# Performance work log

Measured on AMD Instinct MI355X. Metric: run time of the kernel, lower is better.

The kernel has to match this reference:

```python
import jax, jax.numpy as jnp
import numpy as np

ND, NT, B = 16384, 16384, 4096
FD, FT, C = 256, 256, 768


def _gat(x_src, x_dst, ei, Ws, Wd, a_s, a_d, b, num_dst, self_loops):
    """PyG GATConv, heads=1: per-edge attention softmax over incoming edges."""
    if self_loops:
        loops = jnp.arange(num_dst, dtype=ei.dtype)
        ei = jnp.concatenate([ei, jnp.stack([loops, loops])], axis=1)
    src, dst = ei[0], ei[1]
    hs = x_src @ Ws                                   # [Ns, C]
    hd = x_dst @ Wd                                   # [Ndst, C]
    e = jax.nn.leaky_relu((hs @ a_s)[src] + (hd @ a_d)[dst], 0.2)   # [E]
    m = jax.ops.segment_max(e, dst, num_segments=num_dst)
    p = jnp.exp(e - m[dst])
    s = jax.ops.segment_sum(p, dst, num_segments=num_dst)
    alpha = p / (s[dst] + 1e-16)
    out = jax.ops.segment_sum(hs[src] * alpha[:, None], dst, num_segments=num_dst)
    return out + b


def _l2norm(x):
    n = jnp.linalg.norm(x, axis=1, keepdims=True)
    return x / jnp.maximum(n, 1e-12)


def setup_inputs() -> dict:
    ks = iter(jax.random.split(jax.random.key(0), 64))
    def nrm(shape, fan_in=None):
        s = 1.0 if fan_in is None else (1.0 / fan_in) ** 0.5
        return jax.random.normal(next(ks), shape, jnp.float32) * s
    inp = {}
    inp["x_drug"] = nrm((ND, FD))
    inp["x_target"] = nrm((NT, FT))
    inp["cell_features"] = nrm((B, 890))
    for et, fs, fd in (("dd", FD, FD), ("dt", FD, FT), ("tt", FT, FT)):
        inp[f"W_src_{et}"] = nrm((fs, C), fs)
        inp[f"W_dst_{et}"] = nrm((fd, C), fd)
        inp[f"a_src_{et}"] = nrm((C,), C)
        inp[f"a_dst_{et}"] = nrm((C,), C)
        inp[f"b_{et}"] = jnp.zeros((C,), jnp.float32)
    for name, fi, fo in (("red1", 890, 2048), ("red2", 2048, 512), ("red3", 512, 2 * C),
                         ("r2a", 4 * C, 2048), ("r2b", 2048, 512), ("r2c", 512, C), ("cls", C, 2)):
        inp[f"{name}_w"] = nrm((fi, fo), fi)
        inp[f"{name}_b"] = jnp.zeros((fo,), jnp.float32)
    inp["drug1_id"] = jax.random.randint(next(ks), (B,), 0, ND)
    inp["drug2_id"] = jax.random.randint(next(ks), (B,), 0, ND)
    inp["ei_dd"] = jax.random.randint(next(ks), (2, 131072), 0, ND)
    inp["ei_dt"] = jnp.stack([jax.random.randint(next(ks), (262144,), 0, ND),
                              jax.random.randint(next(ks), (262144,), 0, NT)])
    inp["ei_tt"] = jax.random.randint(next(ks), (2, 262144), 0, NT)
    return inp


def reference(x_drug, x_target, cell_features,
              W_src_dd, W_dst_dd, a_src_dd, a_dst_dd, b_dd,
              W_src_dt, W_dst_dt, a_src_dt, a_dst_dt, b_dt,
              W_src_tt, W_dst_tt, a_src_tt, a_dst_tt, b_tt,
              red1_w, red1_b, red2_w, red2_b, red3_w, red3_b,
              r2a_w, r2a_b, r2b_w, r2b_b, r2c_w, r2c_b,
              cls_w, cls_b,
              drug1_id, drug2_id, ei_dd, ei_dt, ei_tt):
    # HeteroConv (aggr='sum') followed by per-type ReLU, num_layers=1
    drug = jax.nn.relu(_gat(x_drug, x_drug, ei_dd,
                            W_src_dd, W_dst_dd, a_src_dd, a_dst_dd, b_dd, ND, True))
    target = jax.nn.relu(
        _gat(x_drug, x_target, ei_dt, W_src_dt, W_dst_dt, a_src_dt, a_dst_dt, b_dt, NT, False)
        + _gat(x_target, x_target, ei_tt, W_src_tt, W_dst_tt, a_src_tt, a_dst_tt, b_tt, NT, True))
    del target  # with num_layers=1 the target embeddings never feed the output (faithful)
    d1 = drug[drug1_id]
    d2 = drug[drug2_id]
    cell = _l2norm(cell_features)
    cell = jax.nn.relu(cell @ red1_w + red1_b)
    cell = jax.nn.relu(cell @ red2_w + red2_b)
    cell = jax.nn.relu(cell @ red3_w + red3_b)          # [B, 2*C]
    hidden = _l2norm(jnp.concatenate([d1, d2, cell], axis=1))  # [B, 4*C]
    hidden = jax.nn.relu(hidden @ r2a_w + r2a_b)
    hidden = jax.nn.relu(hidden @ r2b_w + r2b_b)
    hidden = jax.nn.relu(hidden @ r2c_w + r2c_b)
    return hidden @ cls_w + cls_b                       # [B, 2]
```

## Files before the change

### kernel.cpp

```cpp
#include <hip/hip_runtime.h>
#include <cstdint>

#define ND 16384
#define BATCH 4096
#define CDIM 768
#define E_DD 131072
#define FD 256

typedef unsigned short u16;
typedef u16 u16x4 __attribute__((ext_vector_type(4)));
typedef u16 u16x8 __attribute__((ext_vector_type(8)));
typedef short s16x8 __attribute__((ext_vector_type(8)));
typedef float f32x4 __attribute__((ext_vector_type(4)));

__device__ __forceinline__ u16 f2bf(float x) {
  union { float f; uint32_t u; } v; v.f = x;
  uint32_t r = v.u + 0x7fffu + ((v.u >> 16) & 1u);
  return (u16)(r >> 16);
}
__device__ __forceinline__ float bf2f(u16 h) {
  union { float f; uint32_t u; } v; v.u = ((uint32_t)h) << 16;
  return v.f;
}
__device__ __forceinline__ uint32_t split2p(float x) {
  u16 h = f2bf(x);
  u16 l = f2bf(x - bf2f(h));
  return ((uint32_t)h << 16) | l;
}

#define KP 40

template <int KS, int OUT_BF16, int RELU, int BIAS, int ASPLIT, int ALO, int BLO>
__device__ __forceinline__ void gemm_core(
    int bx, int by, int bz,
    const float* __restrict__ Af,
    const u16* __restrict__ Ahi, const u16* __restrict__ Alo,
    const u16* __restrict__ Bhi, const u16* __restrict__ Blo,
    const float* __restrict__ bias,
    float* __restrict__ Cf, u16* __restrict__ Chi,
    int M, int N, int K, u16* AsB, u16* BsB) {
  constexpr int MT = 4, NT = 4;
  constexpr int BM = 128, BN = 128;
  constexpr int ASEG = BM / 64;
  constexpr int BSEG = BN / 64;

  const int t = threadIdx.x;
  const int bm0 = bx * BM, bn0 = by * BN;
  const int wid = t >> 6, lane = t & 63;
  const int quad = lane >> 4, l16 = lane & 15;
  const int wm0 = (wid >> 1) * (MT * 16);
  const int wn0 = (wid & 1) * (NT * 16);

  const int chunk = K / KS;
  const int kbeg = (KS > 1) ? bz * chunk : 0;
  const int kend = kbeg + chunk;

  auto As = [&](int a, int r, int k) -> u16& { return AsB[(a * BM + r) * KP + k]; };
  auto Bs = [&](int a, int r, int k) -> u16& { return BsB[(a * BN + r) * KP + k]; };

  f32x4 acc[MT][NT];
#pragma unroll
  for (int i = 0; i < MT; ++i)
#pragma unroll
    for (int j = 0; j < NT; ++j) acc[i][j] = (f32x4){0.f, 0.f, 0.f, 0.f};

  u16x8 pAh[ASEG], pAl[ASEG], pBh[BSEG], pBl[BSEG];

  auto loadA = [&](int c, int kk) {
    int s = t + 256 * c, row = s >> 2, kq = (s & 3) * 8;
    size_t off = (size_t)(bm0 + row) * K + kk + kq;
    if (ASPLIT) {
      f32x4 v0 = *(const f32x4*)(Af + off);
      f32x4 v1 = *(const f32x4*)(Af + off + 4);
      u16x8 h, l;
#pragma unroll
      for (int e = 0; e < 4; ++e) {
        uint32_t p = split2p(v0[e]);
        h[e] = (u16)(p >> 16); l[e] = (u16)(p & 0xffffu);
        uint32_t q = split2p(v1[e]);
        h[e + 4] = (u16)(q >> 16); l[e + 4] = (u16)(q & 0xffffu);
      }
      pAh[c] = h; pAl[c] = l;
    } else {
      pAh[c] = *(const u16x8*)(Ahi + off);
      if (ALO) pAl[c] = *(const u16x8*)(Alo + off);
    }
  };
  auto loadB = [&](int c, int kk) {
    int s = t + 256 * c, row = s >> 2, kq = (s & 3) * 8;
    size_t off = (size_t)(bn0 + row) * K + kk + kq;
    pBh[c] = *(const u16x8*)(Bhi + off);
    if (BLO) pBl[c] = *(const u16x8*)(Blo + off);
  };

#pragma unroll
  for (int c = 0; c < ASEG; ++c) loadA(c, kbeg);
#pragma unroll
  for (int c = 0; c < BSEG; ++c) loadB(c, kbeg);

  for (int k0 = kbeg;;) {
    __syncthreads();
#pragma unroll
    for (int c = 0; c < ASEG; ++c) {
      int s = t + 256 * c, row = s >> 2, kq = (s & 3) * 8;
      *(u16x8*)&As(0, row, kq) = pAh[c];
      if (ALO) *(u16x8*)&As(1, row, kq) = pAl[c];
    }
#pragma unroll
    for (int c = 0; c < BSEG; ++c) {
      int s = t + 256 * c, row = s >> 2, kq = (s & 3) * 8;
      *(u16x8*)&Bs(0, row, kq) = pBh[c];
      if (BLO) *(u16x8*)&Bs(1, row, kq) = pBl[c];
    }
    __syncthreads();

    int kn = k0 + 32;
    if (kn < kend) {
#pragma unroll
      for (int c = 0; c < ASEG; ++c) loadA(c, kn);
#pragma unroll
      for (int c = 0; c < BSEG; ++c) loadB(c, kn);
    }

    s16x8 ah[MT], al[MT], bh[NT], bl[NT];
#pragma unroll
    for (int mi = 0; mi < MT; ++mi) {
      ah[mi] = *(const s16x8*)&As(0, wm0 + mi * 16 + l16, quad * 8);
      if (ALO) al[mi] = *(const s16x8*)&As(1, wm0 + mi * 16 + l16, quad * 8);
    }
#pragma unroll
    for (int ni = 0; ni < NT; ++ni) {
      bh[ni] = *(const s16x8*)&Bs(0, wn0 + ni * 16 + l16, quad * 8);
      if (BLO) bl[ni] = *(const s16x8*)&Bs(1, wn0 + ni * 16 + l16, quad * 8);
    }
#pragma unroll
    for (int mi = 0; mi < MT; ++mi)
#pragma unroll
      for (int ni = 0; ni < NT; ++ni) {
        acc[mi][ni] = __builtin_amdgcn_mfma_f32_16x16x32_bf16(
            ah[mi], bh[ni], acc[mi][ni], 0, 0, 0);
        if (BLO)
          acc[mi][ni] = __builtin_amdgcn_mfma_f32_16x16x32_bf16(
              ah[mi], bl[ni], acc[mi][ni], 0, 0, 0);
        if (ALO)
          acc[mi][ni] = __builtin_amdgcn_mfma_f32_16x16x32_bf16(
              al[mi], bh[ni], acc[mi][ni], 0, 0, 0);
      }
    k0 = kn;
    if (k0 >= kend) break;
  }

  float* Cp = (KS > 1) ? Cf + (size_t)bz * M * N : Cf;
#pragma unroll
  for (int mi = 0; mi < MT; ++mi) {
#pragma unroll
    for (int ni = 0; ni < NT; ++ni) {
      int row = bm0 + wm0 + mi * 16 + quad * 4;
      int col = bn0 + wn0 + ni * 16 + l16;
      float bv = BIAS ? bias[col] : 0.f;
#pragma unroll
      for (int r = 0; r < 4; ++r) {
        float v = acc[mi][ni][r] + bv;
        if (RELU) v = fmaxf(v, 0.f);
        size_t o = (size_t)(row + r) * N + col;
        if (OUT_BF16) Chi[o] = f2bf(v);
        else Cp[o] = v;
      }
    }
  }
}

template <int KS, int OUT_BF16, int RELU, int BIAS, int ASPLIT, int ALO, int BLO>
__global__ __launch_bounds__(256) void mfma_gemm(
    const float* __restrict__ Af,
    const u16* __restrict__ Ahi, const u16* __restrict__ Alo,
    const u16* __restrict__ Bhi, const u16* __restrict__ Blo,
    const float* __restrict__ bias,
    float* __restrict__ Cf, u16* __restrict__ Chi,
    int M, int N, int K) {
  __shared__ __align__(16) u16 AsB[(ALO ? 2 : 1) * 128 * KP];
  __shared__ __align__(16) u16 BsB[(BLO ? 2 : 1) * 128 * KP];
  gemm_core<KS, OUT_BF16, RELU, BIAS, ASPLIT, ALO, BLO>(
      blockIdx.x, blockIdx.y, (KS > 1) ? (int)blockIdx.z : 0,
      Af, Ahi, Alo, Bhi, Blo, bias, Cf, Chi, M, N, K, AsB, BsB);
}

__global__ __launch_bounds__(256) void dual_gemm_red1_hs(
    const u16* __restrict__ cn, const u16* __restrict__ r1T,
    const float* __restrict__ red1_b, u16* __restrict__ c1,
    const float* __restrict__ xd, const u16* __restrict__ wsrcT,
    u16* __restrict__ hs) {
  __shared__ __align__(16) u16 AsB[2 * 128 * KP];
  __shared__ __align__(16) u16 BsB[128 * KP];
  int b = blockIdx.x;
  if (b < 512) {
    gemm_core<1, 1, 1, 1, 0, 0, 0>(b & 31, b >> 5, 0, nullptr, cn, nullptr,
                                   r1T, nullptr, red1_b, nullptr, c1,
                                   BATCH, 2048, 896, AsB, BsB);
  } else {
    int b2 = b - 512;
    gemm_core<1, 1, 0, 0, 1, 1, 0>(b2 & 127, b2 >> 7, 0, xd, nullptr, nullptr,
                                   wsrcT, nullptr, nullptr, nullptr, hs,
                                   ND, CDIM, FD, AsB, BsB);
  }
}

template <int KS>
__global__ void reduce_split_ks(const float* __restrict__ P,
                                const float* __restrict__ bias,
                                u16* __restrict__ Chi, int M, int N) {
  int i = blockIdx.x * 256 + threadIdx.x;
  int total = (M * N) >> 2;
  if (i >= total) return;
  f32x4 s = ((const f32x4*)P)[i];
#pragma unroll
  for (int z = 1; z < KS; ++z) s += ((const f32x4*)P)[(size_t)z * total + i];
  int col = (i * 4) % N;
  f32x4 bv = *(const f32x4*)(bias + col);
  u16x4 h;
#pragma unroll
  for (int e = 0; e < 4; ++e) h[e] = f2bf(fmaxf(s[e] + bv[e], 0.f));
  *(u16x4*)&Chi[i * 4] = h;
}

__global__ void reduce_cls(const float* __restrict__ P,
                           const float* __restrict__ bias,
                           const float* __restrict__ clsw,
                           const float* __restrict__ clsb,
                           float* __restrict__ out) {
  int row = blockIdx.x * 4 + (threadIdx.x >> 6);
  int lane = threadIdx.x & 63;
  const f32x4* p0 = (const f32x4*)(P + (size_t)row * CDIM);
  const f32x4* p1 = (const f32x4*)(P + (size_t)BATCH * CDIM + (size_t)row * CDIM);
  float s0 = 0.f, s1 = 0.f;
#pragma unroll
  for (int i = 0; i < 3; ++i) {
    int c4 = lane + 64 * i;
    f32x4 a = p0[c4] + p1[c4];
    f32x4 bv = *(const f32x4*)(bias + c4 * 4);
#pragma unroll
    for (int e = 0; e < 4; ++e) {
      float h = fmaxf(a[e] + bv[e], 0.f);
      int c = c4 * 4 + e;
      s0 = fmaf(h, clsw[c * 2 + 0], s0);
      s1 = fmaf(h, clsw[c * 2 + 1], s1);
    }
  }
#pragma unroll
  for (int m = 32; m; m >>= 1) {
    s0 += __shfl_xor(s0, m);
    s1 += __shfl_xor(s1, m);
  }
  if (lane == 0) {
    out[row * 2 + 0] = s0 + clsb[0];
    out[row * 2 + 1] = s1 + clsb[1];
  }
}

struct TDesc {
  const float* W;
  u16* Th;
  int K, N, Kpad, start;
};
struct TPack { TDesc d[7]; };

__global__ void multi_transpose(TPack p) {
  __shared__ float tile[32][33];
  int b = blockIdx.x;
  int mi = 0;
#pragma unroll
  for (int i = 1; i < 7; ++i)
    if (b >= p.d[i].start) mi = i;
  TDesc dd = p.d[mi];
  int rel = b - dd.start;
  int tilesX = dd.Kpad / 32;
  int k0 = (rel % tilesX) * 32, n0 = (rel / tilesX) * 32;
  int tx = threadIdx.x, ty = threadIdx.y;
#pragma unroll
  for (int i = 0; i < 4; ++i) {
    int k = k0 + ty + 8 * i, n = n0 + tx;
    tile[ty + 8 * i][tx] = (k < dd.K && n < dd.N) ? dd.W[(size_t)k * dd.N + n] : 0.f;
  }
  __syncthreads();
#pragma unroll
  for (int i = 0; i < 4; ++i) {
    int n = n0 + ty + 8 * i, k = k0 + tx;
    if (n < dd.N) dd.Th[(size_t)n * dd.Kpad + k] = f2bf(tile[tx][ty + 8 * i]);
  }
}

__global__ void wvec_kernel(const float* __restrict__ Wsrc,
                            const float* __restrict__ Wdst,
                            const float* __restrict__ a_s,
                            const float* __restrict__ a_d,
                            float* __restrict__ wsv, float* __restrict__ wdv) {
  int k = blockIdx.x;
  int t = threadIdx.x;
  __shared__ float rs[256], rd[256];
  float s = 0.f, d = 0.f;
  for (int c = t; c < CDIM; c += 256) {
    s += Wsrc[(size_t)k * CDIM + c] * a_s[c];
    d += Wdst[(size_t)k * CDIM + c] * a_d[c];
  }
  rs[t] = s; rd[t] = d;
  __syncthreads();
  for (int st = 128; st; st >>= 1) {
    if (t < st) { rs[t] += rs[t + st]; rd[t] += rd[t + st]; }
    __syncthreads();
  }
  if (t == 0) { wsv[k] = rs[0]; wdv[k] = rd[0]; }
}

__global__ void esed_kernel(const float* __restrict__ x,
                            const float* __restrict__ wsv,
                            const float* __restrict__ wdv,
                            float* __restrict__ es, float* __restrict__ ed) {
  int i = blockIdx.x * 256 + threadIdx.x;
  int lane = threadIdx.x & 63;
  int row = i >> 6;
  int c4 = lane * 4;
  f32x4 v = ((const f32x4*)x)[i];
  f32x4 ws = *(const f32x4*)(wsv + c4);
  f32x4 wd = *(const f32x4*)(wdv + c4);
  float a = v[0] * ws[0] + v[1] * ws[1] + v[2] * ws[2] + v[3] * ws[3];
  float b = v[0] * wd[0] + v[1] * wd[1] + v[2] * wd[2] + v[3] * wd[3];
#pragma unroll
  for (int m = 32; m; m >>= 1) {
    a += __shfl_xor(a, m);
    b += __shfl_xor(b, m);
  }
  if (lane == 0) { es[row] = a; ed[row] = b; }
}

__global__ void init_csr(int* counts, int* mask, int* cnt) {
  int i = blockIdx.x * 256 + threadIdx.x;
  if (i < ND) { counts[i] = 1; mask[i] = 0; }
  if (i == 0) *cnt = 0;
}
__global__ void mark_kernel(const int* __restrict__ d1, const int* __restrict__ d2,
                            int* mask) {
  int i = blockIdx.x * 256 + threadIdx.x;
  if (i < BATCH) {
    mask[d1[i]] = 1;
    mask[d2[i]] = 1;
  }
}
__global__ void compact_kernel(const int* __restrict__ mask, int* cnt, int* list) {
  int i = blockIdx.x * 256 + threadIdx.x;
  if (i < ND && mask[i]) {
    int pos = atomicAdd(cnt, 1);
    list[pos] = i;
  }
}

__global__ void count_edges(const int* __restrict__ dst, int* counts) {
  int e = blockIdx.x * 256 + threadIdx.x;
  if (e < E_DD) atomicAdd(&counts[dst[e]], 1);
}
__global__ void scan_kernel(const int* __restrict__ counts, int* __restrict__ offsets,
                            int* __restrict__ cursor, int* __restrict__ slots) {
  __shared__ int part[512];
  int t = threadIdx.x;
  int base = t * 32;
  int s = 0;
  for (int i = 0; i < 32; ++i) s += counts[base + i];
  part[t] = s;
  __syncthreads();
  if (t == 0) {
    int run = 0;
    for (int i = 0; i < 512; ++i) { int tmp = part[i]; part[i] = run; run += tmp; }
    offsets[ND] = run;
  }
  __syncthreads();
  int run = part[t];
  for (int i = 0; i < 32; ++i) {
    int d = base + i;
    offsets[d] = run;
    slots[run] = d;
    cursor[d] = run + 1;
    run += counts[d];
  }
}
__global__ void scatter_edges(const int* __restrict__ src, const int* __restrict__ dst,
                              int* cursor, int* slots) {
  int e = blockIdx.x * 256 + threadIdx.x;
  if (e < E_DD) {
    int pos = atomicAdd(&cursor[dst[e]], 1);
    slots[pos] = src[e];
  }
}

__global__ __launch_bounds__(256) void gat_aggregate(
    const u16* __restrict__ hs, const float* __restrict__ es,
    const float* __restrict__ ed, const int* __restrict__ offsets,
    const int* __restrict__ slots, const float* __restrict__ bias,
    const int* __restrict__ list, const int* __restrict__ cnt,
    u16* __restrict__ out) {
  int idx = blockIdx.x * 4 + (threadIdx.x >> 6);
  if (idx >= *cnt) return;
  int d = list[idx];
  int lane = threadIdx.x & 63;
  int beg = offsets[d], end = offsets[d + 1];
  float edv = ed[d];
  float mx = -1e30f;
  for (int j = beg + lane; j < end; j += 64) {
    float e = es[slots[j]] + edv;
    e = e >= 0.f ? e : 0.2f * e;
    mx = fmaxf(mx, e);
  }
#pragma unroll
  for (int m = 32; m; m >>= 1) mx = fmaxf(mx, __shfl_xor(mx, m));
  float sm = 0.f;
  for (int j = beg + lane; j < end; j += 64) {
    float e = es[slots[j]] + edv;
    e = e >= 0.f ? e : 0.2f * e;
    sm += expf(e - mx);
  }
#pragma unroll
  for (int m = 32; m; m >>= 1) sm += __shfl_xor(sm, m);
  float inv = 1.f / (sm + 1e-16f);
  int c8 = lane * 8;
  int c4 = 512 + lane * 4;
  float a8[8] = {};
  float a4[4] = {};
  for (int j = beg; j < end; ++j) {
    int srcn = slots[j];
    float e = es[srcn] + edv;
    e = e >= 0.f ? e : 0.2f * e;
    float alpha = expf(e - mx) * inv;
    const u16* hrow = hs + (size_t)srcn * CDIM;
    u16x8 r8 = *(const u16x8*)(hrow + c8);
    u16x4 r4 = *(const u16x4*)(hrow + c4);
#pragma unroll
    for (int e2 = 0; e2 < 8; ++e2) a8[e2] = fmaf(alpha, bf2f(r8[e2]), a8[e2]);
#pragma unroll
    for (int e2 = 0; e2 < 4; ++e2) a4[e2] = fmaf(alpha, bf2f(r4[e2]), a4[e2]);
  }
  u16* orow = out + (size_t)d * CDIM;
  u16x8 o8;
  u16x4 o4;
#pragma unroll
  for (int e2 = 0; e2 < 8; ++e2) o8[e2] = f2bf(fmaxf(a8[e2] + bias[c8 + e2], 0.f));
#pragma unroll
  for (int e2 = 0; e2 < 4; ++e2) o4[e2] = f2bf(fmaxf(a4[e2] + bias[c4 + e2], 0.f));
  *(u16x8*)(orow + c8) = o8;
  *(u16x4*)(orow + c4) = o4;
}

__global__ void l2norm_bf16(const float* __restrict__ in, u16* __restrict__ hi,
                            int L, int Lp) {
  int row = blockIdx.x;
  int t = threadIdx.x;
  __shared__ float red[256];
  const float* irow = in + (size_t)row * L;
  float s = 0.f;
  for (int c = t; c < L; c += 256) { float v = irow[c]; s += v * v; }
  red[t] = s;
  __syncthreads();
  for (int st = 128; st; st >>= 1) {
    if (t < st) red[t] += red[t + st];
    __syncthreads();
  }
  float inv = 1.f / fmaxf(sqrtf(red[0]), 1e-12f);
  for (int c = t; c < Lp; c += 256) {
    float v = (c < L) ? irow[c] * inv : 0.f;
    hi[(size_t)row * Lp + c] = f2bf(v);
  }
}

__global__ __launch_bounds__(256) void hidden_build_bf16(
    const u16* __restrict__ drug, const u16* __restrict__ c3,
    const int* __restrict__ d1, const int* __restrict__ d2,
    u16* __restrict__ hhi) {
  int row = blockIdx.x;
  int t = threadIdx.x;
  const u16* s1 = drug + (size_t)d1[row] * CDIM;
  const u16* s2 = drug + (size_t)d2[row] * CDIM;
  const u16* s3 = c3 + (size_t)row * (2 * CDIM);
  float vals[12];
  float ss = 0.f;
#pragma unroll
  for (int i = 0; i < 12; ++i) {
    int c = t + 256 * i;
    float v;
    if (i < 3)      v = bf2f(s1[c]);
    else if (i < 6) v = bf2f(s2[c - CDIM]);
    else            v = bf2f(s3[c - 2 * CDIM]);
    vals[i] = v;
    ss += v * v;
  }
  __shared__ float red[256];
  red[t] = ss;
  __syncthreads();
  for (int st = 128; st; st >>= 1) {
    if (t < st) red[t] += red[t + st];
    __syncthreads();
  }
  float inv = 1.f / fmaxf(sqrtf(red[0]), 1e-12f);
  u16* hrow_h = hhi + (size_t)row * (4 * CDIM);
#pragma unroll
  for (int i = 0; i < 12; ++i) hrow_h[t + 256 * i] = f2bf(vals[i] * inv);
}

extern "C" void kernel_launch(void* const* d_in, const int* in_sizes, int n_in,
                              void* d_out, int out_size, void* d_ws, size_t ws_size,
                              hipStream_t stream) {
  const float* x_drug   = (const float*)d_in[0];
  const float* cellf    = (const float*)d_in[2];
  const float* W_src_dd = (const float*)d_in[3];
  const float* W_dst_dd = (const float*)d_in[4];
  const float* a_src_dd = (const float*)d_in[5];
  const float* a_dst_dd = (const float*)d_in[6];
  const float* b_dd     = (const float*)d_in[7];
  const float* red1_w = (const float*)d_in[18];
  const float* red1_b = (const float*)d_in[19];
  const float* red2_w = (const float*)d_in[20];
  const float* red2_b = (const float*)d_in[21];
  const float* red3_w = (const float*)d_in[22];
  const float* red3_b = (const float*)d_in[23];
  const float* r2a_w  = (const float*)d_in[24];
  const float* r2a_b  = (const float*)d_in[25];
  const float* r2b_w  = (const float*)d_in[26];
  const float* r2b_b  = (const float*)d_in[27];
  const float* r2c_w  = (const float*)d_in[28];
  const float* r2c_b  = (const float*)d_in[29];
  const float* cls_w  = (const float*)d_in[30];
  const float* cls_b  = (const float*)d_in[31];
  const int* drug1_id = (const int*)d_in[32];
  const int* drug2_id = (const int*)d_in[33];
  const int* ei_dd    = (const int*)d_in[34];
  float* out = (float*)d_out;

  const int* dd_src = ei_dd;
  const int* dd_dst = ei_dd + E_DD;

  char* w = (char*)d_ws;
  size_t off = 0;
  auto alloc = [&](size_t bytes) -> char* {
    char* p = w + off;
    off = (off + bytes + 255) & ~(size_t)255;
    return p;
  };
  u16* hs   = (u16*)alloc((size_t)ND * CDIM * 2);
  u16* drug = (u16*)alloc((size_t)ND * CDIM * 2);
  u16* c3   = (u16*)alloc((size_t)BATCH * 2 * CDIM * 2);
  float* P  = (float*)alloc((size_t)4 * BATCH * 512 * 4);
  u16* hid_hi = hs;
  u16* cn_hi = (u16*)alloc((size_t)BATCH * 896 * 2);
  u16* c1_hi = (u16*)alloc((size_t)BATCH * 2048 * 2);
  u16* c2_hi = (u16*)alloc((size_t)BATCH * 512 * 2);
  u16* wsrcT_hi = (u16*)alloc((size_t)CDIM * FD * 2);
  u16* r1T_hi = (u16*)alloc((size_t)2048 * 896 * 2);
  u16* r2T_hi = (u16*)alloc((size_t)512 * 2048 * 2);
  u16* r3T_hi = (u16*)alloc((size_t)1536 * 512 * 2);
  u16* raT_hi = (u16*)alloc((size_t)2048 * 3072 * 2);
  u16* rbT_hi = (u16*)alloc((size_t)512 * 2048 * 2);
  u16* rcT_hi = (u16*)alloc((size_t)768 * 512 * 2);
  float* es  = (float*)alloc((size_t)ND * 4);
  float* ed  = (float*)alloc((size_t)ND * 4);
  float* wsv = (float*)alloc(FD * 4);
  float* wdv = (float*)alloc(FD * 4);
  int* counts  = (int*)alloc((size_t)ND * 4);
  int* offsets = (int*)alloc((size_t)(ND + 1) * 4);
  int* cursor  = (int*)alloc((size_t)ND * 4);
  int* slots   = (int*)alloc((size_t)(E_DD + ND) * 4);
  int* mask    = (int*)alloc((size_t)ND * 4);
  int* list    = (int*)alloc((size_t)ND * 4);
  int* cnt     = (int*)alloc(256);
  (void)ws_size; (void)n_in; (void)in_sizes; (void)out_size;

  TPack tp;
  tp.d[0] = {W_src_dd, wsrcT_hi, 256, 768, 256, 0};
  tp.d[1] = {red1_w, r1T_hi, 890, 2048, 896, 192};
  tp.d[2] = {red2_w, r2T_hi, 2048, 512, 2048, 1984};
  tp.d[3] = {red3_w, r3T_hi, 512, 1536, 512, 3008};
  tp.d[4] = {r2a_w, raT_hi, 3072, 2048, 3072, 3776};
  tp.d[5] = {r2b_w, rbT_hi, 2048, 512, 2048, 9920};
  tp.d[6] = {r2c_w, rcT_hi, 512, 768, 512, 10944};
  multi_transpose<<<11328, dim3(32, 8), 0, stream>>>(tp);

  wvec_kernel<<<FD, 256, 0, stream>>>(W_src_dd, W_dst_dd, a_src_dd, a_dst_dd, wsv, wdv);
  esed_kernel<<<ND * FD / 1024, 256, 0, stream>>>(x_drug, wsv, wdv, es, ed);
  init_csr<<<ND / 256, 256, 0, stream>>>(counts, mask, cnt);
  mark_kernel<<<BATCH / 256, 256, 0, stream>>>(drug1_id, drug2_id, mask);
  compact_kernel<<<ND / 256, 256, 0, stream>>>(mask, cnt, list);
  l2norm_bf16<<<BATCH, 256, 0, stream>>>(cellf, cn_hi, 890, 896);

  dual_gemm_red1_hs<<<1280, 256, 0, stream>>>(cn_hi, r1T_hi, red1_b, c1_hi,
                                              x_drug, wsrcT_hi, hs);

  mfma_gemm<4, 0, 0, 0, 0, 0, 0><<<dim3(BATCH / 128, 512 / 128, 4), 256, 0, stream>>>(
      nullptr, c1_hi, nullptr, r2T_hi, nullptr, nullptr, P, nullptr, BATCH, 512, 2048);
  reduce_split_ks<4><<<BATCH * 512 / 1024, 256, 0, stream>>>(P, red2_b, c2_hi, BATCH, 512);
  mfma_gemm<1, 1, 1, 1, 0, 0, 0><<<dim3(BATCH / 128, 1536 / 128), 256, 0, stream>>>(
      nullptr, c2_hi, nullptr, r3T_hi, nullptr, red3_b, nullptr, c3, BATCH, 1536, 512);

  count_edges<<<E_DD / 256, 256, 0, stream>>>(dd_dst, counts);
  scan_kernel<<<1, 512, 0, stream>>>(counts, offsets, cursor, slots);
  scatter_edges<<<E_DD / 256, 256, 0, stream>>>(dd_src, dd_dst, cursor, slots);
  gat_aggregate<<<ND / 4, 256, 0, stream>>>(hs, es, ed, offsets, slots, b_dd, list, cnt, drug);

  hidden_build_bf16<<<BATCH, 256, 0, stream>>>(drug, c3, drug1_id, drug2_id, hid_hi);

  mfma_gemm<1, 1, 1, 1, 0, 0, 0><<<dim3(BATCH / 128, 2048 / 128), 256, 0, stream>>>(
      nullptr, hid_hi, nullptr, raT_hi, nullptr, r2a_b, nullptr, c1_hi, BATCH, 2048, 3072);
  mfma_gemm<4, 0, 0, 0, 0, 0, 0><<<dim3(BATCH / 128, 512 / 128, 4), 256, 0, stream>>>(
      nullptr, c1_hi, nullptr, rbT_hi, nullptr, nullptr, P, nullptr, BATCH, 512, 2048);
  reduce_split_ks<4><<<BATCH * 512 / 1024, 256, 0, stream>>>(P, r2b_b, c2_hi, BATCH, 512);
  mfma_gemm<2, 0, 0, 0, 0, 0, 0><<<dim3(BATCH / 128, CDIM / 128, 2), 256, 0, stream>>>(
      nullptr, c2_hi, nullptr, rcT_hi, nullptr, nullptr, P, nullptr, BATCH, CDIM, 512);
  reduce_cls<<<BATCH / 4, 256, 0, stream>>>(P, r2c_b, cls_w, cls_b, out);
}
```

Before: 483.6 us.

## Stage plain bf16 GEMM tiles via direct global-to-LDS loads with double buffering

For GEMM instantiations without fp32 splitting or low-part operands, tiles are now copied straight from global memory into LDS with global_load_lds. This skips the register round trip, and a double-buffered scheme needs only one barrier per k-step. The LDS layout drops the padding (stride 32 instead of 40), which may add bank conflicts on the fragment reads. Shared memory in the dual kernel is merged into one buffer sized for both paths. There is no explicit wait on the async LDS loads before the barrier, which risks reading data that has not arrived.

```diff
diff --git a/kernel.cpp b/kernel.cpp
--- a/kernel.cpp
+++ b/kernel.cpp
@@ -27,6 +27,11 @@
   u16 l = f2bf(x - bf2f(h));
   return ((uint32_t)h << 16) | l;
 }
+
+#define GLOAD_LDS16(gp, lp)                                                   \
+  __builtin_amdgcn_global_load_lds(                                           \
+      (__attribute__((address_space(1))) void*)(gp),                          \
+      (__attribute__((address_space(3))) void*)(lp), 16, 0, 0)
 
 #define KP 40
 
@@ -43,6 +48,7 @@
   constexpr int BM = 128, BN = 128;
   constexpr int ASEG = BM / 64;
   constexpr int BSEG = BN / 64;
+  constexpr bool DIRECT = (ASPLIT == 0 && ALO == 0 && BLO == 0);
 
   const int t = threadIdx.x;
   const int bm0 = bx * BM, bn0 = by * BN;
@@ -55,99 +61,167 @@
   const int kbeg = (KS > 1) ? bz * chunk : 0;
   const int kend = kbeg + chunk;
 
-  auto As = [&](int a, int r, int k) -> u16& { return AsB[(a * BM + r) * KP + k]; };
-  auto Bs = [&](int a, int r, int k) -> u16& { return BsB[(a * BN + r) * KP + k]; };
-
   f32x4 acc[MT][NT];
 #pragma unroll
   for (int i = 0; i < MT; ++i)
 #pragma unroll
     for (int j = 0; j < NT; ++j) acc[i][j] = (f32x4){0.f, 0.f, 0.f, 0.f};
 
-  u16x8 pAh[ASEG], pAl[ASEG], pBh[BSEG], pBl[BSEG];
-
-  auto loadA = [&](int c, int kk) {
-    int s = t + 256 * c, row = s >> 2, kq = (s & 3) * 8;
-    size_t off = (size_t)(bm0 + row) * K + kk + kq;
-    if (ASPLIT) {
-      f32x4 v0 = *(const f32x4*)(Af + off);
-      f32x4 v1 = *(const f32x4*)(Af + off + 4);
-      u16x8 h, l;
-#pragma unroll
-      for (int e = 0; e < 4; ++e) {
-        uint32_t p = split2p(v0[e]);
-        h[e] = (u16)(p >> 16); l[e] = (u16)(p & 0xffffu);
-        uint32_t q = split2p(v1[e]);
-        h[e + 4] = (u16)(q >> 16); l[e + 4] = (u16)(q & 0xffffu);
-      }
-      pAh[c] = h; pAl[c] = l;
-    } else {
-      pAh[c] = *(const u16x8*)(Ahi + off);
-      if (ALO) pAl[c] = *(const u16x8*)(Alo + off);
+  if constexpr (DIRECT) {
+    auto stage = [&](int buf, int kk) {
+#pragma unroll
+      for (int c = 0; c < ASEG; ++c) {
+        int s = t + 256 * c;
+        size_t goff = (size_t)(bm0 + (s >> 2)) * K + kk + (s & 3) * 8;
+        int lofs = __builtin_amdgcn_readfirstlane(
+            buf * (2 * BM * 32) + 0 * 0 + (wid * 64 + 256 * c) * 8);
+        GLOAD_LDS16(Ahi + goff, AsB + (buf * (BM * 32) + (lofs - buf * (2 * BM * 32))));
+      }
+#pragma unroll
+      for (int c = 0; c < BSEG; ++c) {
+        int s = t + 256 * c;
+        size_t goff = (size_t)(bn0 + (s >> 2)) * K + kk + (s & 3) * 8;
+        int lofs = __builtin_amdgcn_readfirstlane((wid * 64 + 256 * c) * 8);
+        GLOAD_LDS16(Bhi + goff, BsB + buf * (BN * 32) + lofs);
+      }
+    };
+    auto stageA = [&](int buf, int kk) {
+#pragma unroll
+      for (int c = 0; c < ASEG; ++c) {
+        int s = t + 256 * c;
+        size_t goff = (size_t)(bm0 + (s >> 2)) * K + kk + (s & 3) * 8;
+        int lofs = __builtin_amdgcn_readfirstlane((wid * 64 + 256 * c) * 8);
+        GLOAD_LDS16(Ahi + goff, AsB + buf * (BM * 32) + lofs);
+      }
+    };
+    auto stageB = [&](int buf, int kk) {
+#pragma unroll
+      for (int c = 0; c < BSEG; ++c) {
+        int s = t + 256 * c;
+        size_t goff = (size_t)(bn0 + (s >> 2)) * K + kk + (s & 3) * 8;
+        int lofs = __builtin_amdgcn_readfirstlane((wid * 64 + 256 * c) * 8);
+        GLOAD_LDS16(Bhi + goff, BsB + buf * (BN * 32) + lofs);
+      }
+    };
+    (void)stage;
+    stageA(0, kbeg);
+    stageB(0, kbeg);
+    int cur = 0;
+    for (int k0 = kbeg;;) {
+      __syncthreads();
+      int kn = k0 + 32;
+      if (kn < kend) {
+        stageA(cur ^ 1, kn);
+        stageB(cur ^ 1, kn);
+      }
+      const u16* Ab = AsB + cur * (BM * 32);
+      const u16* Bb = BsB + cur * (BN * 32);
+      s16x8 ah[MT], bh[NT];
+#pragma unroll
+      for (int mi = 0; mi < MT; ++mi)
+        ah[mi] = *(const s16x8*)(Ab + (wm0 + mi * 16 + l16) * 32 + quad * 8);
+#pragma unroll
+      for (int ni = 0; ni < NT; ++ni)
+        bh[ni] = *(const s16x8*)(Bb + (wn0 + ni * 16 + l16) * 32 + quad * 8);
+#pragma unroll
+      for (int mi = 0; mi < MT; ++mi)
+#pragma unroll
+        for (int ni = 0; ni < NT; ++ni)
+          acc[mi][ni] = __builtin_amdgcn_mfma_f32_16x16x32_bf16(
+              ah[mi], bh[ni], acc[mi][ni], 0, 0, 0);
+      k0 = kn;
+      cur ^= 1;
+      if (k0 >= kend) break;
     }
-  };
-  auto loadB = [&](int c, int kk) {
-    int s = t + 256 * c, row = s >> 2, kq = (s & 3) * 8;
-    size_t off = (size_t)(bn0 + row) * K + kk + kq;
-    pBh[c] = *(const u16x8*)(Bhi + off);
-    if (BLO) pBl[c] = *(const u16x8*)(Blo + off);
-  };
-
-#pragma unroll
-  for (int c = 0; c < ASEG; ++c) loadA(c, kbeg);
-#pragma unroll
-  for (int c = 0; c < BSEG; ++c) loadB(c, kbeg);
-
-  for (int k0 = kbeg;;) {
-    __syncthreads();
-#pragma unroll
-    for (int c = 0; c < ASEG; ++c) {
+  } else {
+    auto As = [&](int a, int r, int k) -> u16& { return AsB[(a * BM + r) * KP + k]; };
+    auto Bs = [&](int a, int r, int k) -> u16& { return BsB[(a * BN + r) * KP + k]; };
+
+    u16x8 pAh[ASEG], pAl[ASEG], pBh[BSEG], pBl[BSEG];
+
+    auto loadA = [&](int c, int kk) {
       int s = t + 256 * c, row = s >> 2, kq = (s & 3) * 8;
-      *(u16x8*)&As(0, row, kq) = pAh[c];
-      if (ALO) *(u16x8*)&As(1, row, kq) = pAl[c];
+      size_t off = (size_t)(bm0 + row) * K + kk + kq;
+      if (ASPLIT) {
+        f32x4 v0 = *(const f32x4*)(Af + off);
+        f32x4 v1 = *(const f32x4*)(Af + off + 4);
+        u16x8 h, l;
+#pragma unroll
+        for (int e = 0; e < 4; ++e) {
+          uint32_t p = split2p(v0[e]);
+          h[e] = (u16)(p >> 16); l[e] = (u16)(p & 0xffffu);
+          uint32_t q = split2p(v1[e]);
+          h[e + 4] = (u16)(q >> 16); l[e + 4] = (u16)(q & 0xffffu);
+        }
+        pAh[c] = h; pAl[c] = l;
+      } else {
+        pAh[c] = *(const u16x8*)(Ahi + off);
+        if (ALO) pAl[c] = *(const u16x8*)(Alo + off);
+      }
+    };
+    auto loadB = [&](int c, int kk) {
+      int s = t + 256 * c, row = s >> 2, kq = (s & 3) * 8;
+      size_t off = (size_t)(bn0 + row) * K + kk + kq;
+      pBh[c] = *(const u16x8*)(Bhi + off);
+      if (BLO) pBl[c] = *(const u16x8*)(Blo + off);
+    };
+
+#pragma unroll
+    for (int c = 0; c < ASEG; ++c) loadA(c, kbeg);
+#pragma unroll
+    for (int c = 0; c < BSEG; ++c) loadB(c, kbeg);
+
+    for (int k0 = kbeg;;) {
+      __syncthreads();
+#pragma unroll
+      for (int c = 0; c < ASEG; ++c) {
+        int s = t + 256 * c, row = s >> 2, kq = (s & 3) * 8;
+        *(u16x8*)&As(0, row, kq) = pAh[c];
+        if (ALO) *(u16x8*)&As(1, row, kq) = pAl[c];
+      }
+#pragma unroll
+      for (int c = 0; c < BSEG; ++c) {
+        int s = t + 256 * c, row = s >> 2, kq = (s & 3) * 8;
+        *(u16x8*)&Bs(0, row, kq) = pBh[c];
+        if (BLO) *(u16x8*)&Bs(1, row, kq) = pBl[c];
+      }
+      __syncthreads();
+
+      int kn = k0 + 32;
+      if (kn < kend) {
+#pragma unroll
+        for (int c = 0; c < ASEG; ++c) loadA(c, kn);
+#pragma unroll
+        for (int c = 0; c < BSEG; ++c) loadB(c, kn);
+      }
+
+      s16x8 ah[MT], al[MT], bh[NT], bl[NT];
+#pragma unroll
+      for (int mi = 0; mi < MT; ++mi) {
+        ah[mi] = *(const s16x8*)&As(0, wm0 + mi * 16 + l16, quad * 8);
+        if (ALO) al[mi] = *(const s16x8*)&As(1, wm0 + mi * 16 + l16, quad * 8);
+      }
+#pragma unroll
+      for (int ni = 0; ni < NT; ++ni) {
+        bh[ni] = *(const s16x8*)&Bs(0, wn0 + ni * 16 + l16, quad * 8);
+        if (BLO) bl[ni] = *(const s16x8*)&Bs(1, wn0 + ni * 16 + l16, quad * 8);
+      }
+#pragma unroll
+      for (int mi = 0; mi < MT; ++mi)
+#pragma unroll
+        for (int ni = 0; ni < NT; ++ni) {
+          acc[mi][ni] = __builtin_amdgcn_mfma_f32_16x16x32_bf16(
+              ah[mi], bh[ni], acc[mi][ni], 0, 0, 0);
+          if (BLO)
+            acc[mi][ni] = __builtin_amdgcn_mfma_f32_16x16x32_bf16(
+                ah[mi], bl[ni], acc[mi][ni], 0, 0, 0);
+          if (ALO)
+            acc[mi][ni] = __builtin_amdgcn_mfma_f32_16x16x32_bf16(
+                al[mi], bh[ni], acc[mi][ni], 0, 0, 0);
+        }
+      k0 = kn;
+      if (k0 >= kend) break;
     }
-#pragma unroll
-    for (int c = 0; c < BSEG; ++c) {
-      int s = t + 256 * c, row = s >> 2, kq = (s & 3) * 8;
-      *(u16x8*)&Bs(0, row, kq) = pBh[c];
-      if (BLO) *(u16x8*)&Bs(1, row, kq) = pBl[c];
-    }
-    __syncthreads();
-
-    int kn = k0 + 32;
-    if (kn < kend) {
-#pragma unroll
-      for (int c = 0; c < ASEG; ++c) loadA(c, kn);
-#pragma unroll
-      for (int c = 0; c < BSEG; ++c) loadB(c, kn);
-    }
-
-    s16x8 ah[MT], al[MT], bh[NT], bl[NT];
-#pragma unroll
-    for (int mi = 0; mi < MT; ++mi) {
-      ah[mi] = *(const s16x8*)&As(0, wm0 + mi * 16 + l16, quad * 8);
-      if (ALO) al[mi] = *(const s16x8*)&As(1, wm0 + mi * 16 + l16, quad * 8);
-    }
-#pragma unroll
-    for (int ni = 0; ni < NT; ++ni) {
-      bh[ni] = *(const s16x8*)&Bs(0, wn0 + ni * 16 + l16, quad * 8);
-      if (BLO) bl[ni] = *(const s16x8*)&Bs(1, wn0 + ni * 16 + l16, quad * 8);
-    }
-#pragma unroll
-    for (int mi = 0; mi < MT; ++mi)
-#pragma unroll
-      for (int ni = 0; ni < NT; ++ni) {
-        acc[mi][ni] = __builtin_amdgcn_mfma_f32_16x16x32_bf16(
-            ah[mi], bh[ni], acc[mi][ni], 0, 0, 0);
-        if (BLO)
-          acc[mi][ni] = __builtin_amdgcn_mfma_f32_16x16x32_bf16(
-              ah[mi], bl[ni], acc[mi][ni], 0, 0, 0);
-        if (ALO)
-          acc[mi][ni] = __builtin_amdgcn_mfma_f32_16x16x32_bf16(
-              al[mi], bh[ni], acc[mi][ni], 0, 0, 0);
-      }
-    k0 = kn;
-    if (k0 >= kend) break;
   }
 
   float* Cp = (KS > 1) ? Cf + (size_t)bz * M * N : Cf;
@@ -178,8 +252,9 @@
     const float* __restrict__ bias,
     float* __restrict__ Cf, u16* __restrict__ Chi,
     int M, int N, int K) {
-  __shared__ __align__(16) u16 AsB[(ALO ? 2 : 1) * 128 * KP];
-  __shared__ __align__(16) u16 BsB[(BLO ? 2 : 1) * 128 * KP];
+  constexpr bool DIRECT = (ASPLIT == 0 && ALO == 0 && BLO == 0);
+  __shared__ __align__(16) u16 AsB[DIRECT ? 2 * 128 * 32 : (ALO ? 2 : 1) * 128 * KP];
+  __shared__ __align__(16) u16 BsB[DIRECT ? 2 * 128 * 32 : (BLO ? 2 : 1) * 128 * KP];
   gemm_core<KS, OUT_BF16, RELU, BIAS, ASPLIT, ALO, BLO>(
       blockIdx.x, blockIdx.y, (KS > 1) ? (int)blockIdx.z : 0,
       Af, Ahi, Alo, Bhi, Blo, bias, Cf, Chi, M, N, K, AsB, BsB);
@@ -190,18 +265,17 @@
     const float* __restrict__ red1_b, u16* __restrict__ c1,
     const float* __restrict__ xd, const u16* __restrict__ wsrcT,
     u16* __restrict__ hs) {
-  __shared__ __align__(16) u16 AsB[2 * 128 * KP];
-  __shared__ __align__(16) u16 BsB[128 * KP];
+  __shared__ __align__(16) u16 SMEM[16384];
   int b = blockIdx.x;
   if (b < 512) {
     gemm_core<1, 1, 1, 1, 0, 0, 0>(b & 31, b >> 5, 0, nullptr, cn, nullptr,
                                    r1T, nullptr, red1_b, nullptr, c1,
-                                   BATCH, 2048, 896, AsB, BsB);
+                                   BATCH, 2048, 896, SMEM, SMEM + 2 * 128 * 32);
   } else {
     int b2 = b - 512;
     gemm_core<1, 1, 0, 0, 1, 1, 0>(b2 & 127, b2 >> 7, 0, xd, nullptr, nullptr,
                                    wsrcT, nullptr, nullptr, nullptr, hs,
-                                   ND, CDIM, FD, AsB, BsB);
+                                   ND, CDIM, FD, SMEM, SMEM + 2 * 128 * KP);
   }
 }
 
```

Measured after the change: 484.3 us. No clear change (+0.1%).
